# Optimization experiments

Measured on AMD Instinct MI355X. Metric: run time of the kernel, lower is better.

The kernel has to match this reference:

```python
import jax, jax.numpy as jnp
import numpy as np

D_MODEL = 1024
N_HEADS = 16
HEAD_DIM = 64
BATCH = 4
SEQ = 2048


def setup_inputs() -> dict:
    key = jax.random.key(0)
    ks = jax.random.split(key, 5)
    scale = 1.0 / np.sqrt(D_MODEL)
    return {
        "x": jax.random.normal(ks[0], (BATCH, SEQ, D_MODEL), dtype=jnp.float32),
        "Wq": jax.random.normal(ks[1], (D_MODEL, N_HEADS * HEAD_DIM), dtype=jnp.float32) * scale,
        "Wk": jax.random.normal(ks[2], (D_MODEL, N_HEADS * HEAD_DIM), dtype=jnp.float32) * scale,
        "Wv": jax.random.normal(ks[3], (D_MODEL, N_HEADS * HEAD_DIM), dtype=jnp.float32) * scale,
        "Wo": jax.random.normal(ks[4], (N_HEADS * HEAD_DIM, D_MODEL), dtype=jnp.float32) * scale,
        "bo": jnp.zeros((D_MODEL,), dtype=jnp.float32),
    }


def reference(x, Wq, Wk, Wv, Wo, bo):
    B, S, _ = x.shape
    H, Dh = N_HEADS, HEAD_DIM
    # projections -> [B, H, S, Dh]
    q = (x @ Wq).reshape(B, S, H, Dh).transpose(0, 2, 1, 3)
    k = (x @ Wk).reshape(B, S, H, Dh).transpose(0, 2, 1, 3)
    v = (x @ Wv).reshape(B, S, H, Dh).transpose(0, 2, 1, 3)
    score = jnp.einsum("bhsd,bhtd->bhst", q, k) / jnp.sqrt(jnp.float32(Dh))
    causal = jnp.triu(jnp.ones((S, S), dtype=bool), k=1)
    score = jnp.where(causal, -jnp.inf, score)
    attn_probs = jax.nn.softmax(score, axis=-1)
    # dropout is identity in eval mode
    attn = jnp.einsum("bhst,bhtd->bhsd", attn_probs, v)
    out = attn.transpose(0, 2, 1, 3).reshape(B, S, H * Dh)
    out = out @ Wo + bo
    return (out, attn_probs)
```

## Files before the change

### kernel.cpp

```cpp
#include <hip/hip_runtime.h>
#include <hip/hip_bf16.h>

typedef __attribute__((ext_vector_type(8))) short bf16x8;
typedef __attribute__((ext_vector_type(4))) float f32x4;
typedef unsigned short ushort_t;
typedef unsigned int uint_t;

#define AS1 __attribute__((address_space(1)))
#define AS3 __attribute__((address_space(3)))

__device__ __forceinline__ void gload_lds16(const void* g, void* l) {
    __builtin_amdgcn_global_load_lds((const AS1 void*)g, (AS3 void*)l, 16, 0, 0);
}

__device__ __forceinline__ ushort_t f2b(float f) {
    unsigned u = __builtin_bit_cast(unsigned, f);
    unsigned r = (u + 0x7FFFu + ((u >> 16) & 1u)) >> 16;
    return (ushort_t)r;
}

__global__ __launch_bounds__(256) void convert_x_kernel(const float* __restrict__ in,
                                                        ushort_t* __restrict__ out, int n4) {
    int i = blockIdx.x * blockDim.x + threadIdx.x;
    if (i < n4) {
        float4 f = ((const float4*)in)[i];
        ushort4 u;
        u.x = f2b(f.x); u.y = f2b(f.y); u.z = f2b(f.z); u.w = f2b(f.w);
        ((ushort4*)out)[i] = u;
    }
}

__global__ __launch_bounds__(256) void transpose_w_kernel(const float* __restrict__ W,
                                                          ushort_t* __restrict__ WT) {
    __shared__ float t[32][33];
    int n0 = blockIdx.x * 32, k0 = blockIdx.y * 32;
    int tx = threadIdx.x, ty = threadIdx.y;
    for (int i = 0; i < 4; ++i)
        t[ty + i * 8][tx] = W[(size_t)(k0 + ty + i * 8) * 1024 + n0 + tx];
    __syncthreads();
    for (int i = 0; i < 4; ++i)
        WT[(size_t)(n0 + ty + i * 8) * 1024 + k0 + tx] = f2b(t[tx][ty + i * 8]);
}

template <int N, int OUT_BF16>
__global__ __launch_bounds__(256) void gemm_kernel(const ushort_t* __restrict__ A,
                                                   const ushort_t* __restrict__ BT,
                                                   ushort_t* __restrict__ Cb,
                                                   float* __restrict__ Cf,
                                                   const float* __restrict__ bias) {
    const int K = 1024;
    __shared__ ushort_t As[2 * 128 * 32];
    __shared__ ushort_t Bs[2 * 128 * 32];
    int tid = threadIdx.x;
    int wid = tid >> 6, lane = tid & 63;
    int g = lane >> 4, lr = lane & 15;
    int m0 = blockIdx.x * 128, n0 = blockIdx.y * 128;
    int wm = wid >> 1, wn = wid & 1;

    f32x4 acc[4][4] = {};

    int c0 = wid * 2;
    int lrow = lane >> 2;
    int lcol = ((lane & 3) ^ ((lane >> 3) & 3)) * 8;
    const ushort_t* Ag0 = A  + (size_t)(m0 + c0 * 16 + lrow) * K + lcol;
    const ushort_t* Ag1 = A  + (size_t)(m0 + c0 * 16 + 16 + lrow) * K + lcol;
    const ushort_t* Bg0 = BT + (size_t)(n0 + c0 * 16 + lrow) * K + lcol;
    const ushort_t* Bg1 = BT + (size_t)(n0 + c0 * 16 + 16 + lrow) * K + lcol;

    int swzA = ((lr >> 1) & 3) << 4;

    auto stage = [&](int bufi, int kt) {
        char* a0 = (char*)As + bufi * 8192 + c0 * 1024;
        char* b0 = (char*)Bs + bufi * 8192 + c0 * 1024;
        gload_lds16(Ag0 + kt * 32, a0);
        gload_lds16(Ag1 + kt * 32, a0 + 1024);
        gload_lds16(Bg0 + kt * 32, b0);
        gload_lds16(Bg1 + kt * 32, b0 + 1024);
    };

    stage(0, 0);
    __syncthreads();
    int buf = 0;
    for (int kt = 0; kt < K / 32; ++kt) {
        if (kt + 1 < K / 32) stage(buf ^ 1, kt + 1);
        const char* ab = (const char*)As + buf * 8192;
        const char* bb = (const char*)Bs + buf * 8192;
        bf16x8 af[4], bfr[4];
#pragma unroll
        for (int m = 0; m < 4; ++m) {
            int row = wm * 64 + m * 16 + lr;
            af[m] = *(const bf16x8*)(ab + row * 64 + ((g * 16) ^ swzA));
        }
#pragma unroll
        for (int n = 0; n < 4; ++n) {
            int row = wn * 64 + n * 16 + lr;
            bfr[n] = *(const bf16x8*)(bb + row * 64 + ((g * 16) ^ swzA));
        }
#pragma unroll
        for (int m = 0; m < 4; ++m)
#pragma unroll
            for (int n = 0; n < 4; ++n)
                acc[m][n] = __builtin_amdgcn_mfma_f32_16x16x32_bf16(af[m], bfr[n], acc[m][n], 0, 0, 0);
        __syncthreads();
        buf ^= 1;
    }

#pragma unroll
    for (int m = 0; m < 4; ++m)
#pragma unroll
        for (int n = 0; n < 4; ++n) {
            int row0 = m0 + wm * 64 + m * 16 + g * 4;
            int col  = n0 + wn * 64 + n * 16 + lr;
#pragma unroll
            for (int r = 0; r < 4; ++r) {
                float v = acc[m][n][r];
                if (OUT_BF16)
                    Cb[(size_t)(row0 + r) * N + col] = f2b(v);
                else
                    Cf[(size_t)(row0 + r) * N + col] = v + bias[col];
            }
        }
}

__global__ __launch_bounds__(256) void vt_kernel(const ushort_t* __restrict__ Cqkv,
                                                 ushort_t* __restrict__ Vt) {
    int b = blockIdx.z, h = blockIdx.y, st = blockIdx.x;
    __shared__ ushort_t t[64][72];
    const ushort_t* src = Cqkv + (size_t)b * 2048 * 3072 + 2048 + (size_t)h * 64;
    int tid = threadIdx.x;
#pragma unroll
    for (int i = 0; i < 2; ++i) {
        int c = tid + i * 256;
        int sl = c >> 3, dc = (c & 7) * 8;
        *(bf16x8*)&t[sl][dc] = *(const bf16x8*)(src + (size_t)(st * 64 + sl) * 3072 + dc);
    }
    __syncthreads();
#pragma unroll
    for (int i = 0; i < 2; ++i) {
        int c = tid + i * 256;
        int d = c >> 3, sc = (c & 7) * 8;
        bf16x8 v;
#pragma unroll
        for (int j = 0; j < 8; ++j) v[j] = (short)t[sc + j][d];
        *(bf16x8*)(Vt + ((size_t)(b * 16 + h) * 64 + d) * 2048 + st * 64 + sc) = v;
    }
}

__global__ __launch_bounds__(256) void attn_kernel(const ushort_t* __restrict__ Cqkv,
                                                   const ushort_t* __restrict__ Vtg,
                                                   float* __restrict__ Pout,
                                                   ushort_t* __restrict__ Oout) {
    const int S = 2048, DQ = 3072;
    const float C1 = 0.18033688f;
    const float C2 = 5.77078016f;

    int z = (int)blockIdx.x + 32 * (int)blockIdx.y + 512 * (int)blockIdx.z;
    int h = (z >> 5) & 15, b = z >> 9;
    int qt = ((z & 31) + 13 * ((z >> 8) & 7)) & 31;
    int q0 = qt * 64;

    int tid = threadIdx.x, wid = tid >> 6, lane = tid & 63;
    int g = lane >> 4, lr = lane & 15;

    __shared__ ushort_t Ks[2][4096];
    __shared__ ushort_t Vs[2][4096];
    __shared__ ushort_t Pl[4096];
    char* PlB = (char*)Pl + wid * 2048;

    const ushort_t* Qb = Cqkv + (size_t)b * S * DQ + (size_t)h * 64;
    const ushort_t* Kb = Cqkv + (size_t)b * S * DQ + 1024 + (size_t)h * 64;
    const ushort_t* Vb = Vtg + (size_t)((b * 16 + h) * 64) * 2048;
    float* Pbase = Pout + (((size_t)(b * 16 + h)) * S + q0) * S;

    int srow = lane >> 3;
    int scol = ((lane & 7) ^ srow) * 8;

    auto stageK = [&](int bufi, int tt) {
        char* dst = (char*)&Ks[bufi][0] + wid * 1024;
        gload_lds16(Kb + (size_t)(tt * 64 + wid * 8 + srow) * DQ + scol, dst);
        gload_lds16(Kb + (size_t)(tt * 64 + 32 + wid * 8 + srow) * DQ + scol, dst + 4096);
    };
    auto stageV = [&](int bufi, int tt) {
        char* dst = (char*)&Vs[bufi][0] + wid * 1024;
        gload_lds16(Vb + (size_t)(wid * 8 + srow) * 2048 + tt * 64 + scol, dst);
        gload_lds16(Vb + (size_t)(32 + wid * 8 + srow) * 2048 + tt * 64 + scol, dst + 4096);
    };

    bf16x8 qf[2];
    {
        const ushort_t* qp = Qb + (size_t)(q0 + wid * 16 + lr) * DQ + g * 8;
        qf[0] = *(const bf16x8*)qp;
        qf[1] = *(const bf16x8*)(qp + 32);
    }
    int qloc = wid * 16 + lr;

    float psum = 0.f;
    stageK(0, 0);
    __syncthreads();
    int buf = 0;
    for (int tt = 0; tt <= qt; ++tt) {
        if (tt < qt) stageK(buf ^ 1, tt + 1);
        const char* ksb = (const char*)&Ks[buf][0];
#pragma unroll
        for (int nb = 0; nb < 4; ++nb) {
            int row = nb * 16 + lr;
            int x = (row & 7) << 4;
            f32x4 s = {};
            s = __builtin_amdgcn_mfma_f32_16x16x32_bf16(*(const bf16x8*)(ksb + row * 128 + ((g * 16) ^ x)), qf[0], s, 0, 0, 0);
            s = __builtin_amdgcn_mfma_f32_16x16x32_bf16(*(const bf16x8*)(ksb + row * 128 + ((64 + g * 16) ^ x)), qf[1], s, 0, 0, 0);
            if (tt == qt) {
#pragma unroll
                for (int r = 0; r < 4; ++r)
                    if (nb * 16 + g * 4 + r <= qloc) psum += exp2f(fmaf(s[r], C1, -C2));
            } else {
#pragma unroll
                for (int r = 0; r < 4; ++r) psum += exp2f(fmaf(s[r], C1, -C2));
            }
        }
        __syncthreads();
        buf ^= 1;
    }
    psum += __shfl_xor(psum, 16);
    psum += __shfl_xor(psum, 32);
    float lnl2 = __log2f(psum) + C2;

    f32x4 Oacc[4] = {};
    stageK(buf, 0);
    stageV(buf, 0);
    __syncthreads();
    for (int tt = 0; tt <= qt; ++tt) {
        if (tt < qt) { stageK(buf ^ 1, tt + 1); stageV(buf ^ 1, tt + 1); }
        const char* ksb = (const char*)&Ks[buf][0];
        const char* vsb = (const char*)&Vs[buf][0];
        f32x4 p[4];
#pragma unroll
        for (int nb = 0; nb < 4; ++nb) {
            int row = nb * 16 + lr;
            int x = (row & 7) << 4;
            f32x4 s = {};
            s = __builtin_amdgcn_mfma_f32_16x16x32_bf16(*(const bf16x8*)(ksb + row * 128 + ((g * 16) ^ x)), qf[0], s, 0, 0, 0);
            s = __builtin_amdgcn_mfma_f32_16x16x32_bf16(*(const bf16x8*)(ksb + row * 128 + ((64 + g * 16) ^ x)), qf[1], s, 0, 0, 0);
#pragma unroll
            for (int r = 0; r < 4; ++r) {
                float v = exp2f(fmaf(s[r], C1, -lnl2));
                if (tt == qt && (nb * 16 + g * 4 + r > qloc)) v = 0.f;
                p[nb][r] = v;
            }
        }
#pragma unroll
        for (int nb = 0; nb < 4; ++nb)
            *(f32x4*)(Pbase + (size_t)qloc * S + tt * 64 + nb * 16 + g * 4) = p[nb];
#pragma unroll
        for (int nb = 0; nb < 4; ++nb) {
            uint_t w0, w1;
            asm("v_cvt_pk_bf16_f32 %0, %1, %2" : "=v"(w0) : "v"(p[nb][0]), "v"(p[nb][1]));
            asm("v_cvt_pk_bf16_f32 %0, %1, %2" : "=v"(w1) : "v"(p[nb][2]), "v"(p[nb][3]));
            uint2 w; w.x = w0; w.y = w1;
            *(uint2*)(PlB + ((lr * 128 + nb * 32 + g * 8) ^ ((lr & 7) << 4))) = w;
        }
        __builtin_amdgcn_wave_barrier();
#pragma unroll
        for (int kc = 0; kc < 2; ++kc) {
            bf16x8 pf = *(const bf16x8*)(PlB + ((lr * 128 + kc * 64 + g * 16) ^ ((lr & 7) << 4)));
#pragma unroll
            for (int nb = 0; nb < 4; ++nb) {
                int vrow = nb * 16 + lr;
                bf16x8 vf = *(const bf16x8*)(vsb + vrow * 128 + ((kc * 64 + g * 16) ^ ((vrow & 7) << 4)));
                Oacc[nb] = __builtin_amdgcn_mfma_f32_16x16x32_bf16(pf, vf, Oacc[nb], 0, 0, 0);
            }
        }
        asm volatile("s_waitcnt vmcnt(4)" ::: "memory");
        __builtin_amdgcn_s_barrier();
        __builtin_amdgcn_sched_barrier(0);
        buf ^= 1;
    }

    {
        int vsr = tid >> 2, vsc = (tid & 3) * 16;
        float4 zf = {0.f, 0.f, 0.f, 0.f};
        for (int tt = qt + 1; tt < 32; ++tt) {
            float* dst = Pbase + (size_t)vsr * S + tt * 64 + vsc;
#pragma unroll
            for (int j = 0; j < 4; ++j) ((float4*)dst)[j] = zf;
        }
    }

#pragma unroll
    for (int nb = 0; nb < 4; ++nb)
#pragma unroll
        for (int r = 0; r < 4; ++r) {
            int q = q0 + wid * 16 + g * 4 + r;
            Oout[((size_t)b * S + q) * 1024 + h * 64 + nb * 16 + lr] = f2b(Oacc[nb][r]);
        }
}

extern "C" void kernel_launch(void* const* d_in, const int* in_sizes, int n_in,
                              void* d_out, int out_size, void* d_ws, size_t ws_size,
                              hipStream_t stream) {
    const float* x  = (const float*)d_in[0];
    const float* Wq = (const float*)d_in[1];
    const float* Wk = (const float*)d_in[2];
    const float* Wv = (const float*)d_in[3];
    const float* Wo = (const float*)d_in[4];
    const float* bo = (const float*)d_in[5];

    float* out  = (float*)d_out;
    float* Pout = out + (size_t)8388608;

    char* ws = (char*)d_ws;
    ushort_t* xb    = (ushort_t*)(ws);
    ushort_t* wqkv  = (ushort_t*)(ws + (16u << 20));
    ushort_t* wob   = (ushort_t*)(ws + (22u << 20));
    ushort_t* Cqkv  = (ushort_t*)(ws + (24u << 20));
    ushort_t* Vtw   = (ushort_t*)(ws + (72u << 20));
    ushort_t* attnb = (ushort_t*)(ws + (104u << 20));

    convert_x_kernel<<<8192, 256, 0, stream>>>(x, xb, 2097152);
    transpose_w_kernel<<<dim3(32, 32), dim3(32, 8), 0, stream>>>(Wq, wqkv);
    transpose_w_kernel<<<dim3(32, 32), dim3(32, 8), 0, stream>>>(Wk, wqkv + 1024 * 1024);
    transpose_w_kernel<<<dim3(32, 32), dim3(32, 8), 0, stream>>>(Wv, wqkv + 2 * 1024 * 1024);
    transpose_w_kernel<<<dim3(32, 32), dim3(32, 8), 0, stream>>>(Wo, wob);

    gemm_kernel<3072, 1><<<dim3(64, 24), 256, 0, stream>>>(xb, wqkv, Cqkv, nullptr, nullptr);

    vt_kernel<<<dim3(32, 16, 4), 256, 0, stream>>>(Cqkv, Vtw);

    attn_kernel<<<dim3(32, 16, 4), 256, 0, stream>>>(Cqkv, Vtw, Pout, attnb);

    gemm_kernel<1024, 0><<<dim3(64, 8), 256, 0, stream>>>(attnb, wob, nullptr, out, bo);
}
```

Baseline: 485.8 us.

## Pair complementary causal query tiles per block to balance work and share K/V

Each attention block now handles two query tiles, p and 31-p, so every block covers the same number of key tiles under the causal mask. K/V tiles staged into shared memory are reused by both query tiles, and a permutation table spreads the pairs across the grid. The grid shrinks to 1024 blocks and launch bounds request 4 blocks per CU. The cost is double the accumulator registers and possibly fewer concurrent waves to hide latency.

```diff
diff --git a/kernel.cpp b/kernel.cpp
--- a/kernel.cpp
+++ b/kernel.cpp
@@ -8,6 +8,8 @@
 
 #define AS1 __attribute__((address_space(1)))
 #define AS3 __attribute__((address_space(3)))
+
+__constant__ int P4tab[16] = {0, 5, 10, 15, 1, 4, 11, 14, 2, 7, 8, 13, 3, 6, 9, 12};
 
 __device__ __forceinline__ void gload_lds16(const void* g, void* l) {
     __builtin_amdgcn_global_load_lds((const AS1 void*)g, (AS3 void*)l, 16, 0, 0);
@@ -146,130 +148,198 @@
     }
 }
 
-__global__ __launch_bounds__(256) void attn_kernel(const ushort_t* __restrict__ Cqkv,
-                                                   const ushort_t* __restrict__ Vtg,
-                                                   float* __restrict__ Pout,
-                                                   ushort_t* __restrict__ Oout) {
+__global__ __launch_bounds__(256, 4) void attn_kernel(const ushort_t* __restrict__ Cqkv,
+                                                      const ushort_t* __restrict__ Vtg,
+                                                      float* __restrict__ Pout,
+                                                      ushort_t* __restrict__ Oout) {
     const int S = 2048, DQ = 3072;
     const float C1 = 0.18033688f;
     const float C2 = 5.77078016f;
 
-    int z = (int)blockIdx.x + 32 * (int)blockIdx.y + 512 * (int)blockIdx.z;
-    int h = (z >> 5) & 15, b = z >> 9;
-    int qt = ((z & 31) + 13 * ((z >> 8) & 7)) & 31;
-    int q0 = qt * 64;
+    int z = (int)blockIdx.x;
+    int c = z & 255, j = z >> 8;
+    int p = P4tab[(c & 3) * 4 + j];
+    int h = (c >> 2) & 15, b = c >> 6;
+    int qtA = p, qtB = 31 - p;
 
     int tid = threadIdx.x, wid = tid >> 6, lane = tid & 63;
     int g = lane >> 4, lr = lane & 15;
 
-    __shared__ ushort_t Ks[2][4096];
-    __shared__ ushort_t Vs[2][4096];
+    __shared__ ushort_t KV[4][4096];
     __shared__ ushort_t Pl[4096];
     char* PlB = (char*)Pl + wid * 2048;
 
     const ushort_t* Qb = Cqkv + (size_t)b * S * DQ + (size_t)h * 64;
     const ushort_t* Kb = Cqkv + (size_t)b * S * DQ + 1024 + (size_t)h * 64;
     const ushort_t* Vb = Vtg + (size_t)((b * 16 + h) * 64) * 2048;
-    float* Pbase = Pout + (((size_t)(b * 16 + h)) * S + q0) * S;
+    float* PbaseA = Pout + (((size_t)(b * 16 + h)) * S + qtA * 64) * S;
+    float* PbaseB = Pout + (((size_t)(b * 16 + h)) * S + qtB * 64) * S;
 
     int srow = lane >> 3;
     int scol = ((lane & 7) ^ srow) * 8;
 
-    auto stageK = [&](int bufi, int tt) {
-        char* dst = (char*)&Ks[bufi][0] + wid * 1024;
+    auto stageK = [&](int ri, int tt) {
+        char* dst = (char*)&KV[ri][0] + wid * 1024;
         gload_lds16(Kb + (size_t)(tt * 64 + wid * 8 + srow) * DQ + scol, dst);
         gload_lds16(Kb + (size_t)(tt * 64 + 32 + wid * 8 + srow) * DQ + scol, dst + 4096);
     };
-    auto stageV = [&](int bufi, int tt) {
-        char* dst = (char*)&Vs[bufi][0] + wid * 1024;
+    auto stageV = [&](int ri, int tt) {
+        char* dst = (char*)&KV[2 + ri][0] + wid * 1024;
         gload_lds16(Vb + (size_t)(wid * 8 + srow) * 2048 + tt * 64 + scol, dst);
         gload_lds16(Vb + (size_t)(32 + wid * 8 + srow) * 2048 + tt * 64 + scol, dst + 4096);
     };
 
-    bf16x8 qf[2];
+    bf16x8 qfA[2], qfB[2];
     {
-        const ushort_t* qp = Qb + (size_t)(q0 + wid * 16 + lr) * DQ + g * 8;
-        qf[0] = *(const bf16x8*)qp;
-        qf[1] = *(const bf16x8*)(qp + 32);
+        const ushort_t* qa = Qb + (size_t)(qtA * 64 + wid * 16 + lr) * DQ + g * 8;
+        qfA[0] = *(const bf16x8*)qa;
+        qfA[1] = *(const bf16x8*)(qa + 32);
+        const ushort_t* qb2 = Qb + (size_t)(qtB * 64 + wid * 16 + lr) * DQ + g * 8;
+        qfB[0] = *(const bf16x8*)qb2;
+        qfB[1] = *(const bf16x8*)(qb2 + 32);
     }
     int qloc = wid * 16 + lr;
 
-    float psum = 0.f;
+    float psA = 0.f, psB = 0.f;
     stageK(0, 0);
     __syncthreads();
     int buf = 0;
-    for (int tt = 0; tt <= qt; ++tt) {
-        if (tt < qt) stageK(buf ^ 1, tt + 1);
-        const char* ksb = (const char*)&Ks[buf][0];
+    for (int tt = 0; tt <= qtB; ++tt) {
+        if (tt < qtB) stageK(buf ^ 1, tt + 1);
+        const char* ksb = (const char*)&KV[buf][0];
 #pragma unroll
         for (int nb = 0; nb < 4; ++nb) {
             int row = nb * 16 + lr;
             int x = (row & 7) << 4;
-            f32x4 s = {};
-            s = __builtin_amdgcn_mfma_f32_16x16x32_bf16(*(const bf16x8*)(ksb + row * 128 + ((g * 16) ^ x)), qf[0], s, 0, 0, 0);
-            s = __builtin_amdgcn_mfma_f32_16x16x32_bf16(*(const bf16x8*)(ksb + row * 128 + ((64 + g * 16) ^ x)), qf[1], s, 0, 0, 0);
-            if (tt == qt) {
+            bf16x8 k0 = *(const bf16x8*)(ksb + row * 128 + ((g * 16) ^ x));
+            bf16x8 k1 = *(const bf16x8*)(ksb + row * 128 + ((64 + g * 16) ^ x));
+            f32x4 sB = {};
+            sB = __builtin_amdgcn_mfma_f32_16x16x32_bf16(k0, qfB[0], sB, 0, 0, 0);
+            sB = __builtin_amdgcn_mfma_f32_16x16x32_bf16(k1, qfB[1], sB, 0, 0, 0);
+            if (tt == qtB) {
 #pragma unroll
                 for (int r = 0; r < 4; ++r)
-                    if (nb * 16 + g * 4 + r <= qloc) psum += exp2f(fmaf(s[r], C1, -C2));
+                    if (nb * 16 + g * 4 + r <= qloc) psB += exp2f(fmaf(sB[r], C1, -C2));
             } else {
 #pragma unroll
-                for (int r = 0; r < 4; ++r) psum += exp2f(fmaf(s[r], C1, -C2));
+                for (int r = 0; r < 4; ++r) psB += exp2f(fmaf(sB[r], C1, -C2));
+            }
+            if (tt <= qtA) {
+                f32x4 sA = {};
+                sA = __builtin_amdgcn_mfma_f32_16x16x32_bf16(k0, qfA[0], sA, 0, 0, 0);
+                sA = __builtin_amdgcn_mfma_f32_16x16x32_bf16(k1, qfA[1], sA, 0, 0, 0);
+                if (tt == qtA) {
+#pragma unroll
+                    for (int r = 0; r < 4; ++r)
+                        if (nb * 16 + g * 4 + r <= qloc) psA += exp2f(fmaf(sA[r], C1, -C2));
+                } else {
+#pragma unroll
+                    for (int r = 0; r < 4; ++r) psA += exp2f(fmaf(sA[r], C1, -C2));
+                }
             }
         }
         __syncthreads();
         buf ^= 1;
     }
-    psum += __shfl_xor(psum, 16);
-    psum += __shfl_xor(psum, 32);
-    float lnl2 = __log2f(psum) + C2;
-
-    f32x4 Oacc[4] = {};
-    stageK(buf, 0);
-    stageV(buf, 0);
+    psA += __shfl_xor(psA, 16); psA += __shfl_xor(psA, 32);
+    psB += __shfl_xor(psB, 16); psB += __shfl_xor(psB, 32);
+    float lnA = __log2f(psA) + C2;
+    float lnB = __log2f(psB) + C2;
+
+    f32x4 OA[4] = {}, OB[4] = {};
+    stageK(0, 0);
+    stageV(0, 0);
     __syncthreads();
-    for (int tt = 0; tt <= qt; ++tt) {
-        if (tt < qt) { stageK(buf ^ 1, tt + 1); stageV(buf ^ 1, tt + 1); }
-        const char* ksb = (const char*)&Ks[buf][0];
-        const char* vsb = (const char*)&Vs[buf][0];
-        f32x4 p[4];
-#pragma unroll
-        for (int nb = 0; nb < 4; ++nb) {
-            int row = nb * 16 + lr;
-            int x = (row & 7) << 4;
-            f32x4 s = {};
-            s = __builtin_amdgcn_mfma_f32_16x16x32_bf16(*(const bf16x8*)(ksb + row * 128 + ((g * 16) ^ x)), qf[0], s, 0, 0, 0);
-            s = __builtin_amdgcn_mfma_f32_16x16x32_bf16(*(const bf16x8*)(ksb + row * 128 + ((64 + g * 16) ^ x)), qf[1], s, 0, 0, 0);
-#pragma unroll
-            for (int r = 0; r < 4; ++r) {
-                float v = exp2f(fmaf(s[r], C1, -lnl2));
-                if (tt == qt && (nb * 16 + g * 4 + r > qloc)) v = 0.f;
-                p[nb][r] = v;
-            }
-        }
-#pragma unroll
-        for (int nb = 0; nb < 4; ++nb)
-            *(f32x4*)(Pbase + (size_t)qloc * S + tt * 64 + nb * 16 + g * 4) = p[nb];
-#pragma unroll
-        for (int nb = 0; nb < 4; ++nb) {
-            uint_t w0, w1;
-            asm("v_cvt_pk_bf16_f32 %0, %1, %2" : "=v"(w0) : "v"(p[nb][0]), "v"(p[nb][1]));
-            asm("v_cvt_pk_bf16_f32 %0, %1, %2" : "=v"(w1) : "v"(p[nb][2]), "v"(p[nb][3]));
-            uint2 w; w.x = w0; w.y = w1;
-            *(uint2*)(PlB + ((lr * 128 + nb * 32 + g * 8) ^ ((lr & 7) << 4))) = w;
-        }
-        __builtin_amdgcn_wave_barrier();
-#pragma unroll
-        for (int kc = 0; kc < 2; ++kc) {
-            bf16x8 pf = *(const bf16x8*)(PlB + ((lr * 128 + kc * 64 + g * 16) ^ ((lr & 7) << 4)));
+    buf = 0;
+    for (int tt = 0; tt <= qtB; ++tt) {
+        if (tt < qtB) { stageK(buf ^ 1, tt + 1); stageV(buf ^ 1, tt + 1); }
+        const char* ksb = (const char*)&KV[buf][0];
+        const char* vsb = (const char*)&KV[2 + buf][0];
+
+        {
+            f32x4 pv[4];
 #pragma unroll
             for (int nb = 0; nb < 4; ++nb) {
-                int vrow = nb * 16 + lr;
-                bf16x8 vf = *(const bf16x8*)(vsb + vrow * 128 + ((kc * 64 + g * 16) ^ ((vrow & 7) << 4)));
-                Oacc[nb] = __builtin_amdgcn_mfma_f32_16x16x32_bf16(pf, vf, Oacc[nb], 0, 0, 0);
-            }
-        }
-        asm volatile("s_waitcnt vmcnt(4)" ::: "memory");
+                int row = nb * 16 + lr;
+                int x = (row & 7) << 4;
+                f32x4 s = {};
+                s = __builtin_amdgcn_mfma_f32_16x16x32_bf16(*(const bf16x8*)(ksb + row * 128 + ((g * 16) ^ x)), qfB[0], s, 0, 0, 0);
+                s = __builtin_amdgcn_mfma_f32_16x16x32_bf16(*(const bf16x8*)(ksb + row * 128 + ((64 + g * 16) ^ x)), qfB[1], s, 0, 0, 0);
+#pragma unroll
+                for (int r = 0; r < 4; ++r) {
+                    float v = exp2f(fmaf(s[r], C1, -lnB));
+                    if (tt == qtB && (nb * 16 + g * 4 + r > qloc)) v = 0.f;
+                    pv[nb][r] = v;
+                }
+            }
+#pragma unroll
+            for (int nb = 0; nb < 4; ++nb)
+                *(f32x4*)(PbaseB + (size_t)qloc * S + tt * 64 + nb * 16 + g * 4) = pv[nb];
+#pragma unroll
+            for (int nb = 0; nb < 4; ++nb) {
+                uint_t w0, w1;
+                asm("v_cvt_pk_bf16_f32 %0, %1, %2" : "=v"(w0) : "v"(pv[nb][0]), "v"(pv[nb][1]));
+                asm("v_cvt_pk_bf16_f32 %0, %1, %2" : "=v"(w1) : "v"(pv[nb][2]), "v"(pv[nb][3]));
+                uint2 w; w.x = w0; w.y = w1;
+                *(uint2*)(PlB + ((lr * 128 + nb * 32 + g * 8) ^ ((lr & 7) << 4))) = w;
+            }
+            __builtin_amdgcn_wave_barrier();
+#pragma unroll
+            for (int kc = 0; kc < 2; ++kc) {
+                bf16x8 pf = *(const bf16x8*)(PlB + ((lr * 128 + kc * 64 + g * 16) ^ ((lr & 7) << 4)));
+#pragma unroll
+                for (int nb = 0; nb < 4; ++nb) {
+                    int vrow = nb * 16 + lr;
+                    bf16x8 vf = *(const bf16x8*)(vsb + vrow * 128 + ((kc * 64 + g * 16) ^ ((vrow & 7) << 4)));
+                    OB[nb] = __builtin_amdgcn_mfma_f32_16x16x32_bf16(pf, vf, OB[nb], 0, 0, 0);
+                }
+            }
+            __builtin_amdgcn_wave_barrier();
+        }
+
+        if (tt <= qtA) {
+            f32x4 pv[4];
+#pragma unroll
+            for (int nb = 0; nb < 4; ++nb) {
+                int row = nb * 16 + lr;
+                int x = (row & 7) << 4;
+                f32x4 s = {};
+                s = __builtin_amdgcn_mfma_f32_16x16x32_bf16(*(const bf16x8*)(ksb + row * 128 + ((g * 16) ^ x)), qfA[0], s, 0, 0, 0);
+                s = __builtin_amdgcn_mfma_f32_16x16x32_bf16(*(const bf16x8*)(ksb + row * 128 + ((64 + g * 16) ^ x)), qfA[1], s, 0, 0, 0);
+#pragma unroll
+                for (int r = 0; r < 4; ++r) {
+                    float v = exp2f(fmaf(s[r], C1, -lnA));
+                    if (tt == qtA && (nb * 16 + g * 4 + r > qloc)) v = 0.f;
+                    pv[nb][r] = v;
+                }
+            }
+#pragma unroll
+            for (int nb = 0; nb < 4; ++nb)
+                *(f32x4*)(PbaseA + (size_t)qloc * S + tt * 64 + nb * 16 + g * 4) = pv[nb];
+#pragma unroll
+            for (int nb = 0; nb < 4; ++nb) {
+                uint_t w0, w1;
+                asm("v_cvt_pk_bf16_f32 %0, %1, %2" : "=v"(w0) : "v"(pv[nb][0]), "v"(pv[nb][1]));
+                asm("v_cvt_pk_bf16_f32 %0, %1, %2" : "=v"(w1) : "v"(pv[nb][2]), "v"(pv[nb][3]));
+                uint2 w; w.x = w0; w.y = w1;
+                *(uint2*)(PlB + ((lr * 128 + nb * 32 + g * 8) ^ ((lr & 7) << 4))) = w;
+            }
+            __builtin_amdgcn_wave_barrier();
+#pragma unroll
+            for (int kc = 0; kc < 2; ++kc) {
+                bf16x8 pf = *(const bf16x8*)(PlB + ((lr * 128 + kc * 64 + g * 16) ^ ((lr & 7) << 4)));
+#pragma unroll
+                for (int nb = 0; nb < 4; ++nb) {
+                    int vrow = nb * 16 + lr;
+                    bf16x8 vf = *(const bf16x8*)(vsb + vrow * 128 + ((kc * 64 + g * 16) ^ ((vrow & 7) << 4)));
+                    OA[nb] = __builtin_amdgcn_mfma_f32_16x16x32_bf16(pf, vf, OA[nb], 0, 0, 0);
+                }
+            }
+            __builtin_amdgcn_wave_barrier();
+            asm volatile("s_waitcnt vmcnt(8)" ::: "memory");
+        } else {
+            asm volatile("s_waitcnt vmcnt(4)" ::: "memory");
+        }
         __builtin_amdgcn_s_barrier();
         __builtin_amdgcn_sched_barrier(0);
         buf ^= 1;
@@ -278,10 +348,15 @@
     {
         int vsr = tid >> 2, vsc = (tid & 3) * 16;
         float4 zf = {0.f, 0.f, 0.f, 0.f};
-        for (int tt = qt + 1; tt < 32; ++tt) {
-            float* dst = Pbase + (size_t)vsr * S + tt * 64 + vsc;
-#pragma unroll
-            for (int j = 0; j < 4; ++j) ((float4*)dst)[j] = zf;
+        for (int tt = qtA + 1; tt < 32; ++tt) {
+            float* dst = PbaseA + (size_t)vsr * S + tt * 64 + vsc;
+#pragma unroll
+            for (int jj = 0; jj < 4; ++jj) ((float4*)dst)[jj] = zf;
+        }
+        for (int tt = qtB + 1; tt < 32; ++tt) {
+            float* dst = PbaseB + (size_t)vsr * S + tt * 64 + vsc;
+#pragma unroll
+            for (int jj = 0; jj < 4; ++jj) ((float4*)dst)[jj] = zf;
         }
     }
 
@@ -289,8 +364,10 @@
     for (int nb = 0; nb < 4; ++nb)
 #pragma unroll
         for (int r = 0; r < 4; ++r) {
-            int q = q0 + wid * 16 + g * 4 + r;
-            Oout[((size_t)b * S + q) * 1024 + h * 64 + nb * 16 + lr] = f2b(Oacc[nb][r]);
+            int qA = qtA * 64 + wid * 16 + g * 4 + r;
+            int qB = qtB * 64 + wid * 16 + g * 4 + r;
+            Oout[((size_t)b * S + qA) * 1024 + h * 64 + nb * 16 + lr] = f2b(OA[nb][r]);
+            Oout[((size_t)b * S + qB) * 1024 + h * 64 + nb * 16 + lr] = f2b(OB[nb][r]);
         }
 }
 
@@ -325,7 +402,7 @@
 
     vt_kernel<<<dim3(32, 16, 4), 256, 0, stream>>>(Cqkv, Vtw);
 
-    attn_kernel<<<dim3(32, 16, 4), 256, 0, stream>>>(Cqkv, Vtw, Pout, attnb);
+    attn_kernel<<<1024, 256, 0, stream>>>(Cqkv, Vtw, Pout, attnb);
 
     gemm_kernel<1024, 0><<<dim3(64, 8), 256, 0, stream>>>(attnb, wob, nullptr, out, bo);
 }
```

After: 479.0 us. Within noise of the previous version (-1.4%).
